# Kernel optimization log

Measured on AMD Instinct MI355X. Metric: run time of the kernel, lower is better.

Reference implementation:

```python
import jax, jax.numpy as jnp
import numpy as np
import math

B, S, D, H, W = 4, 8192, 1024, 16, 512  # batch, seq, d_model, heads, attention_window
HD = D // H


def setup_inputs() -> dict:
    key = jax.random.key(0)
    ks = jax.random.split(key, 5)
    scale = 0.02
    return {
        "x": jax.random.normal(ks[0], (B, S, D), dtype=jnp.float32),
        "wq": jax.random.normal(ks[1], (D, D), dtype=jnp.float32) * scale,
        "bq": jnp.zeros((D,), dtype=jnp.float32),
        "wk": jax.random.normal(ks[2], (D, D), dtype=jnp.float32) * scale,
        "bk": jnp.zeros((D,), dtype=jnp.float32),
        "wv": jax.random.normal(ks[3], (D, D), dtype=jnp.float32) * scale,
        "bv": jnp.zeros((D,), dtype=jnp.float32),
        "wo": jax.random.normal(ks[4], (D, D), dtype=jnp.float32) * scale,
        "bo": jnp.zeros((D,), dtype=jnp.float32),
    }


def reference(x, wq, bq, wk, bk, wv, bv, wo, bo):
    # torch Linear: y = x @ W.T + b
    q = (x @ wq.T + bq).reshape(B, S, H, HD)
    k = (x @ wk.T + bk).reshape(B, S, H, HD)
    v = (x @ wv.T + bv).reshape(B, S, H, HD)

    nb = S // W  # number of query blocks
    qb = q.reshape(B, nb, W, H, HD)

    # pad keys/values by W at the front so every block sees a 2W key window
    kp = jnp.pad(k, ((0, 0), (W, 0), (0, 0), (0, 0)))
    vp = jnp.pad(v, ((0, 0), (W, 0), (0, 0), (0, 0)))
    # padded key indices for block n: [n*W, n*W + 2W) <-> original [n*W - W, n*W + W)
    idx = jnp.arange(nb)[:, None] * W + jnp.arange(2 * W)[None, :]  # [nb, 2W]
    kb = kp[:, idx]  # [B, nb, 2W, H, HD]
    vb = vp[:, idx]  # [B, nb, 2W, H, HD]

    scores = jnp.einsum('bnqhd,bnkhd->bnhqk', qb, kb) / math.sqrt(HD)
    valid = (idx >= W)  # padded (out-of-range) keys only occur for block 0
    scores = jnp.where(valid[None, :, None, None, :], scores, -jnp.inf)
    attn = jax.nn.softmax(scores, axis=-1)  # softmax over the block's key window

    out = jnp.einsum('bnhqk,bnkhd->bnqhd', attn, vb).reshape(B, S, D)
    return out @ wo.T + bo
```

## Files before the change

kernel.cpp:

```cpp
#include <hip/hip_runtime.h>
#include <hip/hip_bf16.h>
#include <cstdint>

typedef __bf16 bf16;
typedef __attribute__((ext_vector_type(8))) __bf16 bf16x8;
typedef __attribute__((ext_vector_type(4))) __bf16 bf16x4;
typedef __attribute__((ext_vector_type(4))) float f32x4;
typedef __attribute__((ext_vector_type(16))) float f32x16;
typedef __attribute__((ext_vector_type(4))) unsigned int u32x4;

#define B_ 4
#define S_ 8192
#define D_ 1024
#define H_ 16
#define HD_ 64
#define W_ 512
#define M_ (B_*S_)

#define EXP2F(x) __builtin_amdgcn_exp2f(x)
#define MFMA16(a,b,c) __builtin_amdgcn_mfma_f32_16x16x32_bf16(a,b,c,0,0,0)
#define MFMA32(a,b,c) __builtin_amdgcn_mfma_f32_32x32x16_bf16(a,b,c,0,0,0)

__device__ __forceinline__ void async16(const void* g, void* l) {
  __builtin_amdgcn_global_load_lds(
      (const __attribute__((address_space(1))) unsigned int*)g,
      (__attribute__((address_space(3))) unsigned int*)l, 16, 0, 0);
}

__device__ __forceinline__ void cast_region(const float* __restrict__ in,
                                            bf16* __restrict__ out, int n4,
                                            int i0, int stride) {
  for (int i = i0; i < n4; i += stride) {
    f32x4 v = ((const f32x4*)in)[i];
    bf16x4 o = { (bf16)v[0], (bf16)v[1], (bf16)v[2], (bf16)v[3] };
    ((bf16x4*)out)[i] = o;
  }
}

__global__ void cast_all(const float* __restrict__ x,  bf16* __restrict__ xb,
                         const float* __restrict__ wq, bf16* __restrict__ wqb,
                         const float* __restrict__ wk, bf16* __restrict__ wkb,
                         const float* __restrict__ wv, bf16* __restrict__ wvb,
                         const float* __restrict__ wo, bf16* __restrict__ wob) {
  int i0 = blockIdx.x * blockDim.x + threadIdx.x;
  int stride = gridDim.x * blockDim.x;
  cast_region(x,  xb,  M_*D_/4, i0, stride);
  cast_region(wq, wqb, D_*D_/4, i0, stride);
  cast_region(wk, wkb, D_*D_/4, i0, stride);
  cast_region(wv, wvb, D_*D_/4, i0, stride);
  cast_region(wo, wob, D_*D_/4, i0, stride);
}

template<int MODE>
__global__ void __launch_bounds__(512, 2) gemm_bt(
    const bf16* __restrict__ A, const bf16* __restrict__ Bw,
    const float* __restrict__ bias, void* __restrict__ outp, float scale)
{
  constexpr int K = D_, N = D_;
  __shared__ char lds[3 * 32768];
  int bid = blockIdx.x;
  int nid = (bid & 7) * 64 + (bid >> 3);
  int bm = nid >> 2, bn = nid & 3;
  const int tid = threadIdx.x, lane = tid & 63;
  const int w = tid >> 6, wr = w >> 2, wc = w & 3;
  f32x4 acc[8][4] = {};
  const int sR  = ((tid >> 6) * 16) + (tid & 15);
  const int skb = ((tid >> 4) & 3) * 16;
  const char* Ab = (const char*)(A + (size_t)bm * 256 * K);
  const char* Bb = (const char*)(Bw + (size_t)bn * 256 * K);

  auto stageA = [&](int t2, int h) {
    char* dst = lds + (t2 % 3) * 32768 + h * 8192 + tid * 16;
    async16(Ab + (size_t)(h * 128 + sR) * (K * 2) + t2 * 64 + skb, dst);
  };
  auto stageB = [&](int t2, int h) {
    char* dst = lds + (t2 % 3) * 32768 + 16384 + h * 8192 + tid * 16;
    async16(Bb + (size_t)(h * 128 + sR) * (K * 2) + t2 * 64 + skb, dst);
  };

  stageA(0, 0); stageB(0, 0); stageA(0, 1); stageB(0, 1);
  stageA(1, 0); stageB(1, 0); stageA(1, 1); stageB(1, 1);
  asm volatile("s_waitcnt vmcnt(4)" ::: "memory");
  __builtin_amdgcn_s_barrier();

#pragma unroll 1
  for (int t = 0; t < 32; ++t) {
    const char* base = lds + (t % 3) * 32768;
    const char* baseB = base + 16384;
    bool pre = (t < 30);
    if (pre) { stageA(t + 2, 0); stageB(t + 2, 0); }
    bf16x8 a[4], b[4];
#pragma unroll
    for (int mi = 0; mi < 4; ++mi)
      a[mi] = *(const bf16x8*)(base + (wr * 8 + mi) * 1024 + lane * 16);
#pragma unroll
    for (int ni = 0; ni < 4; ++ni)
      b[ni] = *(const bf16x8*)(baseB + (wc * 4 + ni) * 1024 + lane * 16);
    __builtin_amdgcn_s_barrier();
    asm volatile("s_waitcnt lgkmcnt(0)" ::: "memory");
    __builtin_amdgcn_sched_barrier(0);
    __builtin_amdgcn_s_setprio(1);
#pragma unroll
    for (int mi = 0; mi < 4; ++mi)
#pragma unroll
      for (int ni = 0; ni < 4; ++ni)
        acc[mi][ni] = MFMA16(a[mi], b[ni], acc[mi][ni]);
    __builtin_amdgcn_s_setprio(0);
    __builtin_amdgcn_s_barrier();
    if (pre) { stageA(t + 2, 1); stageB(t + 2, 1); }
    bf16x8 a2[4];
#pragma unroll
    for (int mi = 0; mi < 4; ++mi)
      a2[mi] = *(const bf16x8*)(base + (wr * 8 + 4 + mi) * 1024 + lane * 16);
    __builtin_amdgcn_s_barrier();
    asm volatile("s_waitcnt lgkmcnt(0)" ::: "memory");
    __builtin_amdgcn_sched_barrier(0);
    __builtin_amdgcn_s_setprio(1);
#pragma unroll
    for (int mi = 0; mi < 4; ++mi)
#pragma unroll
      for (int ni = 0; ni < 4; ++ni)
        acc[4 + mi][ni] = MFMA16(a2[mi], b[ni], acc[4 + mi][ni]);
    __builtin_amdgcn_s_setprio(0);
    if (pre) {
      asm volatile("s_waitcnt vmcnt(4)" ::: "memory");
    } else {
      asm volatile("s_waitcnt vmcnt(0)" ::: "memory");
    }
    __builtin_amdgcn_s_barrier();
  }

  int row0 = bm * 256 + wr * 128, col0 = bn * 256 + wc * 64;
  int rsub = (lane >> 4) * 4;
#pragma unroll
  for (int ni = 0; ni < 4; ++ni) {
    int col = col0 + ni * 16 + (lane & 15);
    float bz = bias[col];
#pragma unroll
    for (int mi = 0; mi < 8; ++mi) {
#pragma unroll
      for (int r = 0; r < 4; ++r) {
        int row = row0 + mi * 16 + rsub + r;
        float v = (acc[mi][ni][r] + bz) * scale;
        if (MODE == 0) {
          ((bf16*)outp)[(size_t)row * N + col] = (bf16)v;
        } else if (MODE == 1) {
          ((bf16*)outp)[((size_t)(row >> 13) * D_ + col) * S_ + (row & (S_-1))] = (bf16)v;
        } else {
          ((float*)outp)[(size_t)row * N + col] = v;
        }
      }
    }
  }
}

__global__ void __launch_bounds__(256, 3) attn_kernel(
    const bf16* __restrict__ Q, const bf16* __restrict__ Kb,
    const bf16* __restrict__ Vt, bf16* __restrict__ Ao)
{
  __shared__ char Klds[3][8192];
  __shared__ char Vlds[3][8192];
  int x = blockIdx.x;
  int qt = (x >> 3) & 3;
  int g  = (x & 7) + 8 * (x >> 5);
  int h = g & 15, n = (g >> 4) & 15, b = g >> 8;
  int tid = threadIdx.x, lane = tid & 63, w = tid >> 6;
  int hi = lane >> 5, qv = lane & 31;
  int qrow = n * W_ + qt * 128 + w * 32;

  const bf16* Qrow = Q + ((size_t)(b * S_ + qrow + qv)) * D_ + h * 64;
  bf16x8 Qf[4];
#pragma unroll
  for (int s = 0; s < 4; ++s) Qf[s] = *(const bf16x8*)(Qrow + s * 16 + hi * 8);

  const bf16* Kg = Kb + ((size_t)b * S_) * D_ + h * 64;
  const bf16* Vg = Vt + ((size_t)(b * H_ + h) * HD_) * S_;

  const int srow = tid >> 3;
  const int sseg = (tid & 7) ^ (srow & 7);
  const int fswq = (qv & 7) << 4;

  f32x16 O0 = {}, O1 = {};
  float l_r = 0.f;

  const int c0 = (n == 0) ? 8 : 0;
  const int ksbase = (n - 1) * W_;

  auto stage = [&](int c) {
    int ks = ksbase + c * 64;
    int so = (c % 3) * 8192;
    const bf16* kr = Kg + (size_t)(ks + srow) * D_ + sseg * 8;
    async16(kr,                    &Klds[0][0] + so + tid * 16);
    async16(kr + 32 * D_,          &Klds[0][0] + so + 4096 + tid * 16);
    const bf16* vr = Vg + (size_t)srow * S_ + ks + sseg * 8;
    async16(vr,                    &Vlds[0][0] + so + tid * 16);
    async16(vr + (size_t)32 * S_,  &Vlds[0][0] + so + 4096 + tid * 16);
  };

  stage(c0);
  stage(c0 + 1);
  asm volatile("s_waitcnt vmcnt(4)" ::: "memory");
  __builtin_amdgcn_s_barrier();

  for (int c = c0; c < 16; ++c) {
    bool pre = (c + 2 < 16);
    if (pre) stage(c + 2);
    const char* kbuf = &Klds[0][0] + (c % 3) * 8192;
    const char* vbuf = &Vlds[0][0] + (c % 3) * 8192;
    f32x16 C0 = {}, C1 = {};
    __builtin_amdgcn_s_setprio(1);
#pragma unroll
    for (int s = 0; s < 4; ++s) {
      bf16x8 k0 = *(const bf16x8*)(kbuf + qv * 128        + ((s * 32 + hi * 16) ^ fswq));
      bf16x8 k1 = *(const bf16x8*)(kbuf + (32 + qv) * 128 + ((s * 32 + hi * 16) ^ fswq));
      C0 = MFMA32(k0, Qf[s], C0);
      C1 = MFMA32(k1, Qf[s], C1);
    }
    __builtin_amdgcn_s_setprio(0);
    float p0[16], p1[16];
#pragma unroll
    for (int r = 0; r < 16; ++r) {
      p0[r] = EXP2F(C0[r]);
      p1[r] = EXP2F(C1[r]);
    }
    float q0[8], q1[4];
#pragma unroll
    for (int i = 0; i < 8; ++i)
      q0[i] = (p0[2*i] + p0[2*i+1]) + (p1[2*i] + p1[2*i+1]);
#pragma unroll
    for (int i = 0; i < 4; ++i) q1[i] = q0[2*i] + q0[2*i+1];
    l_r += (q1[0] + q1[1]) + (q1[2] + q1[3]);
    unsigned int L0[8], L1[8];
#pragma unroll
    for (int t = 0; t < 8; ++t) {
      asm("v_cvt_pk_bf16_f32 %0, %1, %2" : "=v"(L0[t]) : "v"(p0[2*t]), "v"(p0[2*t+1]));
      asm("v_cvt_pk_bf16_f32 %0, %1, %2" : "=v"(L1[t]) : "v"(p1[2*t]), "v"(p1[2*t+1]));
    }
    asm volatile("v_permlane32_swap_b32 %0, %1" : "+v"(L0[0]), "+v"(L0[2]));
    asm volatile("v_permlane32_swap_b32 %0, %1" : "+v"(L0[1]), "+v"(L0[3]));
    asm volatile("v_permlane32_swap_b32 %0, %1" : "+v"(L0[4]), "+v"(L0[6]));
    asm volatile("v_permlane32_swap_b32 %0, %1" : "+v"(L0[5]), "+v"(L0[7]));
    asm volatile("v_permlane32_swap_b32 %0, %1" : "+v"(L1[0]), "+v"(L1[2]));
    asm volatile("v_permlane32_swap_b32 %0, %1" : "+v"(L1[1]), "+v"(L1[3]));
    asm volatile("v_permlane32_swap_b32 %0, %1" : "+v"(L1[4]), "+v"(L1[6]));
    asm volatile("v_permlane32_swap_b32 %0, %1" : "+v"(L1[5]), "+v"(L1[7]));
    u32x4 F[2][2];
    F[0][0] = u32x4{L0[0], L0[1], L0[2], L0[3]};
    F[0][1] = u32x4{L0[4], L0[5], L0[6], L0[7]};
    F[1][0] = u32x4{L1[0], L1[1], L1[2], L1[3]};
    F[1][1] = u32x4{L1[4], L1[5], L1[6], L1[7]};
    __builtin_amdgcn_s_setprio(1);
#pragma unroll
    for (int T = 0; T < 2; ++T)
#pragma unroll
      for (int s = 0; s < 2; ++s) {
        bf16x8 pf = *(bf16x8*)&F[T][s];
        int kbyteoff = T * 64 + s * 32 + hi * 16;
        bf16x8 v0 = *(const bf16x8*)(vbuf + qv * 128        + (kbyteoff ^ fswq));
        bf16x8 v1 = *(const bf16x8*)(vbuf + (32 + qv) * 128 + (kbyteoff ^ fswq));
        O0 = MFMA32(v0, pf, O0);
        O1 = MFMA32(v1, pf, O1);
      }
    __builtin_amdgcn_s_setprio(0);
    if (pre) {
      asm volatile("s_waitcnt vmcnt(4)" ::: "memory");
    } else {
      asm volatile("s_waitcnt vmcnt(0)" ::: "memory");
    }
    __builtin_amdgcn_s_barrier();
  }
  float lt = l_r + __shfl_xor(l_r, 32);
  float inv = 1.0f / lt;
  size_t obase = ((size_t)(b * S_ + qrow + qv)) * D_ + h * 64;
#pragma unroll
  for (int ot = 0; ot < 2; ++ot) {
#pragma unroll
    for (int rq = 0; rq < 4; ++rq) {
      int hd = ot * 32 + 8 * rq + 4 * hi;
      bf16x4 ov;
#pragma unroll
      for (int j = 0; j < 4; ++j) {
        float val = (ot == 0 ? O0[rq*4 + j] : O1[rq*4 + j]) * inv;
        ov[j] = (bf16)val;
      }
      *(bf16x4*)(Ao + obase + hd) = ov;
    }
  }
}

extern "C" void kernel_launch(void* const* d_in, const int* in_sizes, int n_in,
                              void* d_out, int out_size, void* d_ws, size_t ws_size,
                              hipStream_t stream) {
  const float* x  = (const float*)d_in[0];
  const float* wq = (const float*)d_in[1];
  const float* bq = (const float*)d_in[2];
  const float* wk = (const float*)d_in[3];
  const float* bk = (const float*)d_in[4];
  const float* wv = (const float*)d_in[5];
  const float* bv = (const float*)d_in[6];
  const float* wo = (const float*)d_in[7];
  const float* bo = (const float*)d_in[8];
  float* out = (float*)d_out;

  char* ws = (char*)d_ws;
  const size_t sz = (size_t)M_ * D_ * 2;
  bf16* xb  = (bf16*)(ws + 0*sz);
  bf16* qb  = (bf16*)(ws + 1*sz);
  bf16* kb  = (bf16*)(ws + 2*sz);
  bf16* vt  = (bf16*)(ws + 3*sz);
  bf16* ao  = (bf16*)(ws + 4*sz);
  bf16* wqb = (bf16*)(ws + 5*sz);
  bf16* wkb = wqb + (size_t)D_*D_;
  bf16* wvb = wkb + (size_t)D_*D_;
  bf16* wob = wvb + (size_t)D_*D_;

  cast_all<<<2048, 256, 0, stream>>>(x, xb, wq, wqb, wk, wkb, wv, wvb, wo, wob);

  gemm_bt<0><<<512, 512, 0, stream>>>(xb, wqb, bq, qb, 0.125f * 1.44269504f);
  gemm_bt<0><<<512, 512, 0, stream>>>(xb, wkb, bk, kb, 1.0f);
  gemm_bt<1><<<512, 512, 0, stream>>>(xb, wvb, bv, vt, 1.0f);

  attn_kernel<<<4096, 256, 0, stream>>>(qb, kb, vt, ao);

  gemm_bt<2><<<512, 512, 0, stream>>>(ao, wob, bo, out, 1.0f);
}
```

Before: 551.0 us.

## Switch GEMM to 32x32 MFMA tiles and double-buffer attention for occupancy

The projection GEMM moves from 16x16x32 to 32x32x16 MFMA with a matching LDS staging layout. It also drops the intra-iteration barriers and lgkmcnt waits, and issues the A and B prefetches at different points in the loop. The attention kernel goes from triple to double buffering of K/V in LDS and raises launch bounds from 3 to 5 blocks per CU, trading prefetch depth for occupancy. Removing the barriers and lgkmcnt waits in the GEMM risks LDS read-after-write hazards with the async loads.

```diff
diff --git a/kernel.cpp b/kernel.cpp
--- a/kernel.cpp
+++ b/kernel.cpp
@@ -18,7 +18,6 @@
 #define M_ (B_*S_)
 
 #define EXP2F(x) __builtin_amdgcn_exp2f(x)
-#define MFMA16(a,b,c) __builtin_amdgcn_mfma_f32_16x16x32_bf16(a,b,c,0,0,0)
 #define MFMA32(a,b,c) __builtin_amdgcn_mfma_f32_32x32x16_bf16(a,b,c,0,0,0)
 
 __device__ __forceinline__ void async16(const void* g, void* l) {
@@ -63,64 +62,62 @@
   int bm = nid >> 2, bn = nid & 3;
   const int tid = threadIdx.x, lane = tid & 63;
   const int w = tid >> 6, wr = w >> 2, wc = w & 3;
-  f32x4 acc[8][4] = {};
-  const int sR  = ((tid >> 6) * 16) + (tid & 15);
-  const int skb = ((tid >> 4) & 3) * 16;
+  f32x16 acc[4][2] = {};
+  const int sr31 = tid & 31;
+  const int skh  = (tid >> 5) & 1;
   const char* Ab = (const char*)(A + (size_t)bm * 256 * K);
   const char* Bb = (const char*)(Bw + (size_t)bn * 256 * K);
 
-  auto stageA = [&](int t2, int h) {
-    char* dst = lds + (t2 % 3) * 32768 + h * 8192 + tid * 16;
-    async16(Ab + (size_t)(h * 128 + sR) * (K * 2) + t2 * 64 + skb, dst);
+  auto stageA = [&](int t2, int j) {
+    int f = j * 8 + (tid >> 6), rf = f >> 1, ks = f & 1;
+    char* dst = lds + (t2 % 3) * 32768 + j * 8192 + tid * 16;
+    async16(Ab + (size_t)(rf * 32 + sr31) * (K * 2) + t2 * 64 + ks * 32 + skh * 16, dst);
   };
-  auto stageB = [&](int t2, int h) {
-    char* dst = lds + (t2 % 3) * 32768 + 16384 + h * 8192 + tid * 16;
-    async16(Bb + (size_t)(h * 128 + sR) * (K * 2) + t2 * 64 + skb, dst);
+  auto stageB = [&](int t2, int j) {
+    int f = j * 8 + (tid >> 6), cf = f >> 1, ks = f & 1;
+    char* dst = lds + (t2 % 3) * 32768 + 16384 + j * 8192 + tid * 16;
+    async16(Bb + (size_t)(cf * 32 + sr31) * (K * 2) + t2 * 64 + ks * 32 + skh * 16, dst);
   };
 
-  stageA(0, 0); stageB(0, 0); stageA(0, 1); stageB(0, 1);
-  stageA(1, 0); stageB(1, 0); stageA(1, 1); stageB(1, 1);
+  stageA(0, 0); stageA(0, 1); stageB(0, 0); stageB(0, 1);
+  stageA(1, 0); stageA(1, 1); stageB(1, 0); stageB(1, 1);
   asm volatile("s_waitcnt vmcnt(4)" ::: "memory");
   __builtin_amdgcn_s_barrier();
 
 #pragma unroll 1
   for (int t = 0; t < 32; ++t) {
-    const char* base = lds + (t % 3) * 32768;
+    const char* base  = lds + (t % 3) * 32768;
     const char* baseB = base + 16384;
     bool pre = (t < 30);
-    if (pre) { stageA(t + 2, 0); stageB(t + 2, 0); }
-    bf16x8 a[4], b[4];
-#pragma unroll
-    for (int mi = 0; mi < 4; ++mi)
-      a[mi] = *(const bf16x8*)(base + (wr * 8 + mi) * 1024 + lane * 16);
-#pragma unroll
-    for (int ni = 0; ni < 4; ++ni)
-      b[ni] = *(const bf16x8*)(baseB + (wc * 4 + ni) * 1024 + lane * 16);
-    __builtin_amdgcn_s_barrier();
-    asm volatile("s_waitcnt lgkmcnt(0)" ::: "memory");
-    __builtin_amdgcn_sched_barrier(0);
+    if (pre) { stageA(t + 2, 0); stageA(t + 2, 1); }
+    bf16x8 a0[4], b0[2];
+#pragma unroll
+    for (int rb = 0; rb < 4; ++rb)
+      a0[rb] = *(const bf16x8*)(base + ((wr * 4 + rb) * 2 + 0) * 1024 + lane * 16);
+#pragma unroll
+    for (int cb = 0; cb < 2; ++cb)
+      b0[cb] = *(const bf16x8*)(baseB + ((wc * 2 + cb) * 2 + 0) * 1024 + lane * 16);
     __builtin_amdgcn_s_setprio(1);
 #pragma unroll
-    for (int mi = 0; mi < 4; ++mi)
-#pragma unroll
-      for (int ni = 0; ni < 4; ++ni)
-        acc[mi][ni] = MFMA16(a[mi], b[ni], acc[mi][ni]);
+    for (int rb = 0; rb < 4; ++rb)
+#pragma unroll
+      for (int cb = 0; cb < 2; ++cb)
+        acc[rb][cb] = MFMA32(a0[rb], b0[cb], acc[rb][cb]);
     __builtin_amdgcn_s_setprio(0);
-    __builtin_amdgcn_s_barrier();
-    if (pre) { stageA(t + 2, 1); stageB(t + 2, 1); }
-    bf16x8 a2[4];
-#pragma unroll
-    for (int mi = 0; mi < 4; ++mi)
-      a2[mi] = *(const bf16x8*)(base + (wr * 8 + 4 + mi) * 1024 + lane * 16);
-    __builtin_amdgcn_s_barrier();
-    asm volatile("s_waitcnt lgkmcnt(0)" ::: "memory");
-    __builtin_amdgcn_sched_barrier(0);
+    if (pre) { stageB(t + 2, 0); stageB(t + 2, 1); }
+    bf16x8 a1[4], b1[2];
+#pragma unroll
+    for (int rb = 0; rb < 4; ++rb)
+      a1[rb] = *(const bf16x8*)(base + ((wr * 4 + rb) * 2 + 1) * 1024 + lane * 16);
+#pragma unroll
+    for (int cb = 0; cb < 2; ++cb)
+      b1[cb] = *(const bf16x8*)(baseB + ((wc * 2 + cb) * 2 + 1) * 1024 + lane * 16);
     __builtin_amdgcn_s_setprio(1);
 #pragma unroll
-    for (int mi = 0; mi < 4; ++mi)
-#pragma unroll
-      for (int ni = 0; ni < 4; ++ni)
-        acc[4 + mi][ni] = MFMA16(a2[mi], b[ni], acc[4 + mi][ni]);
+    for (int rb = 0; rb < 4; ++rb)
+#pragma unroll
+      for (int cb = 0; cb < 2; ++cb)
+        acc[rb][cb] = MFMA32(a1[rb], b1[cb], acc[rb][cb]);
     __builtin_amdgcn_s_setprio(0);
     if (pre) {
       asm volatile("s_waitcnt vmcnt(4)" ::: "memory");
@@ -131,17 +128,16 @@
   }
 
   int row0 = bm * 256 + wr * 128, col0 = bn * 256 + wc * 64;
-  int rsub = (lane >> 4) * 4;
-#pragma unroll
-  for (int ni = 0; ni < 4; ++ni) {
-    int col = col0 + ni * 16 + (lane & 15);
+#pragma unroll
+  for (int cb = 0; cb < 2; ++cb) {
+    int col = col0 + cb * 32 + (lane & 31);
     float bz = bias[col];
 #pragma unroll
-    for (int mi = 0; mi < 8; ++mi) {
-#pragma unroll
-      for (int r = 0; r < 4; ++r) {
-        int row = row0 + mi * 16 + rsub + r;
-        float v = (acc[mi][ni][r] + bz) * scale;
+    for (int rb = 0; rb < 4; ++rb) {
+#pragma unroll
+      for (int reg = 0; reg < 16; ++reg) {
+        int row = row0 + rb * 32 + (reg & 3) + 8 * (reg >> 2) + 4 * (lane >> 5);
+        float v = (acc[rb][cb][reg] + bz) * scale;
         if (MODE == 0) {
           ((bf16*)outp)[(size_t)row * N + col] = (bf16)v;
         } else if (MODE == 1) {
@@ -154,12 +150,12 @@
   }
 }
 
-__global__ void __launch_bounds__(256, 3) attn_kernel(
+__global__ void __launch_bounds__(256, 5) attn_kernel(
     const bf16* __restrict__ Q, const bf16* __restrict__ Kb,
     const bf16* __restrict__ Vt, bf16* __restrict__ Ao)
 {
-  __shared__ char Klds[3][8192];
-  __shared__ char Vlds[3][8192];
+  __shared__ char Klds[2][8192];
+  __shared__ char Vlds[2][8192];
   int x = blockIdx.x;
   int qt = (x >> 3) & 3;
   int g  = (x & 7) + 8 * (x >> 5);
@@ -188,7 +184,7 @@
 
   auto stage = [&](int c) {
     int ks = ksbase + c * 64;
-    int so = (c % 3) * 8192;
+    int so = (c & 1) * 8192;
     const bf16* kr = Kg + (size_t)(ks + srow) * D_ + sseg * 8;
     async16(kr,                    &Klds[0][0] + so + tid * 16);
     async16(kr + 32 * D_,          &Klds[0][0] + so + 4096 + tid * 16);
@@ -198,15 +194,14 @@
   };
 
   stage(c0);
-  stage(c0 + 1);
-  asm volatile("s_waitcnt vmcnt(4)" ::: "memory");
+  asm volatile("s_waitcnt vmcnt(0)" ::: "memory");
   __builtin_amdgcn_s_barrier();
 
+#pragma unroll 1
   for (int c = c0; c < 16; ++c) {
-    bool pre = (c + 2 < 16);
-    if (pre) stage(c + 2);
-    const char* kbuf = &Klds[0][0] + (c % 3) * 8192;
-    const char* vbuf = &Vlds[0][0] + (c % 3) * 8192;
+    if (c + 1 < 16) stage(c + 1);
+    const char* kbuf = &Klds[0][0] + (c & 1) * 8192;
+    const char* vbuf = &Vlds[0][0] + (c & 1) * 8192;
     f32x16 C0 = {}, C1 = {};
     __builtin_amdgcn_s_setprio(1);
 #pragma unroll
@@ -223,13 +218,11 @@
       p0[r] = EXP2F(C0[r]);
       p1[r] = EXP2F(C1[r]);
     }
-    float q0[8], q1[4];
+    float q0[8];
 #pragma unroll
     for (int i = 0; i < 8; ++i)
       q0[i] = (p0[2*i] + p0[2*i+1]) + (p1[2*i] + p1[2*i+1]);
-#pragma unroll
-    for (int i = 0; i < 4; ++i) q1[i] = q0[2*i] + q0[2*i+1];
-    l_r += (q1[0] + q1[1]) + (q1[2] + q1[3]);
+    l_r += ((q0[0] + q0[1]) + (q0[2] + q0[3])) + ((q0[4] + q0[5]) + (q0[6] + q0[7]));
     unsigned int L0[8], L1[8];
 #pragma unroll
     for (int t = 0; t < 8; ++t) {
@@ -262,11 +255,7 @@
         O1 = MFMA32(v1, pf, O1);
       }
     __builtin_amdgcn_s_setprio(0);
-    if (pre) {
-      asm volatile("s_waitcnt vmcnt(4)" ::: "memory");
-    } else {
-      asm volatile("s_waitcnt vmcnt(0)" ::: "memory");
-    }
+    asm volatile("s_waitcnt vmcnt(0)" ::: "memory");
     __builtin_amdgcn_s_barrier();
   }
   float lt = l_r + __shfl_xor(l_r, 32);
```

Result: slower. 609.8 us (+10.7%).
